# Optimization experiments

Measured on AMD Instinct MI355X. Metric: run time of the kernel, lower is better.

Reference implementation:

```python
import jax, jax.numpy as jnp
import numpy as np

# column-index constants for the node feature matrix and edge attributes
VM, VA, PG, QG, PD, QD = 0, 1, 2, 3, 4, 5
G_COL, B_COL = 0, 1

N_NODES = 100000
N_EDGES = 3200000
N_FEAT = 6


def setup_inputs() -> dict:
    key = jax.random.key(0)
    k1, k2, k3, k4, k5, k6 = jax.random.split(key, 6)
    pred = jax.random.normal(k1, (N_NODES, N_FEAT), dtype=jnp.float32)
    target = jax.random.normal(k2, (N_NODES, N_FEAT), dtype=jnp.float32)
    src = jax.random.randint(k3, (N_EDGES,), 0, N_NODES, dtype=jnp.int32)
    dst = jax.random.randint(k4, (N_EDGES,), 0, N_NODES, dtype=jnp.int32)
    edge_index = jnp.stack([src, dst], axis=0)
    edge_attr = jax.random.normal(k5, (N_EDGES, 2), dtype=jnp.float32)
    mask = jax.random.bernoulli(k6, 0.5, (N_NODES, N_FEAT))
    return {"pred": pred, "target": target, "edge_index": edge_index,
            "edge_attr": edge_attr, "mask": mask}


def reference(pred, target, edge_index, edge_attr, mask):
    # temp_pred[~mask] = target[~mask]
    tp = jnp.where(mask, pred, target)

    V_m = tp[:, VM]
    V_a = tp[:, VA]
    V = V_m * jnp.exp(1j * V_a)           # complex64 [N]
    V_conj = jnp.conj(V)

    # conj(Y_bus) entries on edges: G - jB
    Y_conj = edge_attr[:, G_COL] - 1j * edge_attr[:, B_COL]  # complex64 [E]

    row, col = edge_index[0], edge_index[1]
    # (Y_bus_conj @ V_conj)[i] = sum over edges (i,j) of conj(Y_ij) * conj(V_j)
    msg = Y_conj * V_conj[col]                               # gather-multiply [E]
    matvec = jax.ops.segment_sum(msg, row, num_segments=tp.shape[0])  # scatter-add [N]

    S_injection = V * matvec                                  # diag(V) @ (...)

    net_P = tp[:, PG] - tp[:, PD]
    net_Q = tp[:, QG] - tp[:, QD]
    diff = (net_P + 1j * net_Q) - S_injection

    loss = jnp.mean(jnp.abs(diff))
    real_loss = jnp.mean(jnp.abs(jnp.real(diff)))
    imag_loss = jnp.mean(jnp.abs(jnp.imag(diff)))
    return (loss, real_loss, imag_loss)
```

## Files before the change

### kernel.cpp

```cpp
#include <hip/hip_runtime.h>
#include <hip/hip_fp16.h>
#include <math.h>

constexpr int N_NODES = 100000;
constexpr int N_EDGES = 3200000;
constexpr int NF      = 6;

constexpr int BSHIFT  = 10;
constexpr int BNODES  = 1 << BSHIFT;
constexpr int NB      = (N_NODES + BNODES - 1) >> BSHIFT;
constexpr int CAP     = 33792;
constexpr int NSLICE  = 16;
constexpr int TILE    = 2048;
constexpr int EPT     = TILE / 256;
constexpr int NBLK_PART = (N_EDGES + TILE - 1) / TILE;
constexpr int VPREP_BLOCKS = (N_NODES + 255) / 256;

constexpr size_t OFF_V    = 0;
constexpr size_t OFF_REC  = OFF_V  + (size_t)N_NODES * 8;
constexpr size_t OFF_PART = OFF_REC + (size_t)NB * CAP * 8;
constexpr size_t OFF_CNT  = OFF_PART + (size_t)NB * NSLICE * BNODES * 8;
constexpr size_t WS_NEED  = OFF_CNT + 1024;

union F2U { float2 f; unsigned long long u; };

__device__ __forceinline__ float2 half2u_to_f2(unsigned u) {
    __half2 h;
    *reinterpret_cast<unsigned*>(&h) = u;
    return __half22float2(h);
}

__global__ __launch_bounds__(256) void partition_edges(
        const int* __restrict__ row, const int* __restrict__ col,
        const float2* __restrict__ attr,
        const float* __restrict__ pred, const float* __restrict__ target,
        const unsigned char* __restrict__ mask,
        float2* __restrict__ v_out,
        unsigned int* __restrict__ gcur,
        uint2* __restrict__ rec_g) {
    __shared__ unsigned int h[4][NB];
    __shared__ unsigned int cur[4][NB];
    __shared__ int wb[4][NB];
    __shared__ int dbase[NB];
    __shared__ unsigned int tot_s[NB];
    __shared__ uint2 rec_s[TILE];
    __shared__ unsigned char bkt_s[TILE];
    __shared__ int total_s;

    const int tid = threadIdx.x;
    const int w = tid >> 6;
    const int e0 = blockIdx.x * TILE;
    const int e_base = e0 + tid * EPT;
    const bool ok = e_base < N_EDGES;

    if (blockIdx.x < VPREP_BLOCKS) {
        int i = blockIdx.x * 256 + tid;
        if (i < N_NODES) {
            const int bb = i * NF;
            float vm = mask[bb + 0] ? pred[bb + 0] : target[bb + 0];
            float va = mask[bb + 1] ? pred[bb + 1] : target[bb + 1];
            float sn, cs;
            sincosf(va, &sn, &cs);
            v_out[i] = make_float2(vm * cs, vm * sn);
        }
    }

    for (int i = tid; i < 4 * NB; i += 256) {
        (&h[0][0])[i] = 0u;
        (&cur[0][0])[i] = 0u;
    }
    __syncthreads();

    int r[EPT];
    if (ok) {
        int4 ra = *(const int4*)(row + e_base);
        int4 rb = *(const int4*)(row + e_base + 4);
        r[0]=ra.x; r[1]=ra.y; r[2]=ra.z; r[3]=ra.w;
        r[4]=rb.x; r[5]=rb.y; r[6]=rb.z; r[7]=rb.w;
        #pragma unroll
        for (int k = 0; k < EPT; ++k)
            atomicAdd(&h[w][r[k] >> BSHIFT], 1u);
    }
    __syncthreads();

    if (tid < NB)
        tot_s[tid] = h[0][tid] + h[1][tid] + h[2][tid] + h[3][tid];
    __syncthreads();

    if (tid < NB) {
        int lbase = 0;
        for (int j = 0; j < tid; ++j) lbase += (int)tot_s[j];
        unsigned t0 = h[0][tid], t1 = h[1][tid], t2 = h[2][tid];
        unsigned tot = tot_s[tid];
        unsigned g = tot ? atomicAdd(&gcur[tid], tot) : 0u;
        dbase[tid] = (int)g - lbase;
        wb[0][tid] = lbase;
        wb[1][tid] = lbase + (int)t0;
        wb[2][tid] = lbase + (int)(t0 + t1);
        wb[3][tid] = lbase + (int)(t0 + t1 + t2);
        if (tid == NB - 1) total_s = lbase + (int)tot;
    }
    __syncthreads();

    if (ok) {
        int4 ca = *(const int4*)(col + e_base);
        int4 cb = *(const int4*)(col + e_base + 4);
        int c[EPT] = {ca.x, ca.y, ca.z, ca.w, cb.x, cb.y, cb.z, cb.w};
        float4 a0 = *(const float4*)(attr + e_base);
        float4 a1 = *(const float4*)(attr + e_base + 2);
        float4 a2 = *(const float4*)(attr + e_base + 4);
        float4 a3 = *(const float4*)(attr + e_base + 6);
        float gx[EPT] = {a0.x, a0.z, a1.x, a1.z, a2.x, a2.z, a3.x, a3.z};
        float gy[EPT] = {a0.y, a0.w, a1.y, a1.w, a2.y, a2.w, a3.y, a3.w};
        #pragma unroll
        for (int k = 0; k < EPT; ++k) {
            int rr = r[k];
            int b = rr >> BSHIFT;
            int slot = wb[w][b] + (int)atomicAdd(&cur[w][b], 1u);
            __half2 hh = __floats2half2_rn(gx[k], gy[k]);
            rec_s[slot] = make_uint2(
                (unsigned)c[k] | ((unsigned)(rr & (BNODES - 1)) << 17),
                *reinterpret_cast<unsigned int*>(&hh));
            bkt_s[slot] = (unsigned char)b;
        }
    }
    __syncthreads();

    const int total = total_s;
    for (int j = tid; j < total; j += 256) {
        int b = (int)bkt_s[j];
        int g = dbase[b] + j;
        if (g < CAP)
            rec_g[(size_t)b * CAP + g] = rec_s[j];
    }
}

__global__ __launch_bounds__(256) void accum_finalize(
        const unsigned int* __restrict__ gcur,
        const uint2* __restrict__ rec,
        unsigned long long* __restrict__ partials,
        unsigned int* __restrict__ sdone,
        float* __restrict__ sums,
        unsigned int* __restrict__ done_all,
        const float* __restrict__ pred,
        const float* __restrict__ target,
        const unsigned char* __restrict__ mask,
        const float2* __restrict__ v,
        float* __restrict__ out) {
    __shared__ float acc_re[BNODES];
    __shared__ float acc_im[BNODES];
    __shared__ unsigned int old_s;
    const int tid = threadIdx.x;
    const int b = blockIdx.x / NSLICE;
    const int s = blockIdx.x % NSLICE;
    int cnt = (int)min(gcur[b], (unsigned)CAP);
    for (int i = tid; i < BNODES; i += 256) { acc_re[i] = 0.f; acc_im[i] = 0.f; }
    __syncthreads();
    int per = (((cnt + NSLICE - 1) / NSLICE) + 3) & ~3;
    int st = s * per;
    int en = min(st + per, cnt);
    const uint2* rp = rec + (size_t)b * CAP;
    int j = st + 4 * tid;
    for (; j + 3 < en; j += 1024) {
        uint4 q0 = *(const uint4*)(rp + j);
        uint4 q1 = *(const uint4*)(rp + j + 2);
        int c0 = (int)(q0.x & 0x1FFFFu), li0 = (int)(q0.x >> 17);
        int c1 = (int)(q0.z & 0x1FFFFu), li1 = (int)(q0.z >> 17);
        int c2 = (int)(q1.x & 0x1FFFFu), li2 = (int)(q1.x >> 17);
        int c3 = (int)(q1.z & 0x1FFFFu), li3 = (int)(q1.z >> 17);
        float2 vv0 = v[c0];
        float2 vv1 = v[c1];
        float2 vv2 = v[c2];
        float2 vv3 = v[c3];
        float2 gb0 = half2u_to_f2(q0.y);
        float2 gb1 = half2u_to_f2(q0.w);
        float2 gb2 = half2u_to_f2(q1.y);
        float2 gb3 = half2u_to_f2(q1.w);
        atomicAdd(&acc_re[li0], fmaf(gb0.x, vv0.x, -gb0.y * vv0.y));
        atomicAdd(&acc_im[li0], -fmaf(gb0.x, vv0.y, gb0.y * vv0.x));
        atomicAdd(&acc_re[li1], fmaf(gb1.x, vv1.x, -gb1.y * vv1.y));
        atomicAdd(&acc_im[li1], -fmaf(gb1.x, vv1.y, gb1.y * vv1.x));
        atomicAdd(&acc_re[li2], fmaf(gb2.x, vv2.x, -gb2.y * vv2.y));
        atomicAdd(&acc_im[li2], -fmaf(gb2.x, vv2.y, gb2.y * vv2.x));
        atomicAdd(&acc_re[li3], fmaf(gb3.x, vv3.x, -gb3.y * vv3.y));
        atomicAdd(&acc_im[li3], -fmaf(gb3.x, vv3.y, gb3.y * vv3.x));
    }
    for (; j < en; ++j) {
        uint2 q = rp[j];
        int c0 = (int)(q.x & 0x1FFFFu), li0 = (int)(q.x >> 17);
        float2 vv0 = v[c0];
        float2 gb0 = half2u_to_f2(q.y);
        atomicAdd(&acc_re[li0], fmaf(gb0.x, vv0.x, -gb0.y * vv0.y));
        atomicAdd(&acc_im[li0], -fmaf(gb0.x, vv0.y, gb0.y * vv0.x));
    }
    __syncthreads();
    unsigned long long* p = partials + ((size_t)b * NSLICE + s) * BNODES;
    for (int i = tid; i < BNODES; i += 256) {
        F2U cvt;
        cvt.f = make_float2(acc_re[i], acc_im[i]);
        __hip_atomic_store(&p[i], cvt.u, __ATOMIC_RELAXED, __HIP_MEMORY_SCOPE_AGENT);
    }
    asm volatile("s_waitcnt vmcnt(0)" ::: "memory");
    __syncthreads();
    if (tid == 0)
        old_s = __hip_atomic_fetch_add(&sdone[b], 1u, __ATOMIC_RELAXED,
                                       __HIP_MEMORY_SCOPE_AGENT);
    __syncthreads();
    if (old_s != (unsigned)(NSLICE - 1)) return;

    const unsigned long long* pb = partials + (size_t)b * NSLICE * BNODES;
    float a = 0.f, ar = 0.f, ai = 0.f;
    for (int li = tid; li < BNODES; li += 256) {
        int i = (b << BSHIFT) + li;
        if (i >= N_NODES) break;
        float mr = 0.f, mi = 0.f;
        #pragma unroll
        for (int s2 = 0; s2 < NSLICE; ++s2) {
            F2U cvt;
            cvt.u = __hip_atomic_load(&pb[(size_t)s2 * BNODES + li],
                                      __ATOMIC_RELAXED, __HIP_MEMORY_SCOPE_AGENT);
            mr += cvt.f.x; mi += cvt.f.y;
        }
        const int bb = i * NF;
        float pg = mask[bb + 2] ? pred[bb + 2] : target[bb + 2];
        float qg = mask[bb + 3] ? pred[bb + 3] : target[bb + 3];
        float pd = mask[bb + 4] ? pred[bb + 4] : target[bb + 4];
        float qd = mask[bb + 5] ? pred[bb + 5] : target[bb + 5];
        float netP = pg - pd;
        float netQ = qg - qd;
        float2 vv = v[i];
        float s_re = vv.x * mr - vv.y * mi;
        float s_im = vv.x * mi + vv.y * mr;
        float dre = netP - s_re;
        float dim = netQ - s_im;
        ar += fabsf(dre);
        ai += fabsf(dim);
        a  += sqrtf(dre * dre + dim * dim);
    }
    #pragma unroll
    for (int off = 32; off > 0; off >>= 1) {
        a  += __shfl_down(a,  off, 64);
        ar += __shfl_down(ar, off, 64);
        ai += __shfl_down(ai, off, 64);
    }
    __shared__ float red[3][4];
    int wave = tid >> 6;
    int lane = tid & 63;
    if (lane == 0) { red[0][wave] = a; red[1][wave] = ar; red[2][wave] = ai; }
    __syncthreads();
    if (tid == 0) {
        float r0 = atomicAdd(&sums[0], red[0][0] + red[0][1] + red[0][2] + red[0][3]);
        float r1 = atomicAdd(&sums[1], red[1][0] + red[1][1] + red[1][2] + red[1][3]);
        float r2 = atomicAdd(&sums[2], red[2][0] + red[2][1] + red[2][2] + red[2][3]);
        float chk = r0 + r1 + r2;
        if (chk == chk) {
            unsigned fin = atomicAdd(done_all, 1u);
            if (fin == (unsigned)(NB - 1)) {
                const float inv = 1.0f / (float)N_NODES;
                float t0 = atomicAdd(&sums[0], 0.f);
                float t1 = atomicAdd(&sums[1], 0.f);
                float t2 = atomicAdd(&sums[2], 0.f);
                __hip_atomic_store(&out[0], t0 * inv, __ATOMIC_RELAXED, __HIP_MEMORY_SCOPE_AGENT);
                __hip_atomic_store(&out[1], t1 * inv, __ATOMIC_RELAXED, __HIP_MEMORY_SCOPE_AGENT);
                __hip_atomic_store(&out[2], t2 * inv, __ATOMIC_RELAXED, __HIP_MEMORY_SCOPE_AGENT);
            }
        }
    }
}

__global__ void node_prep_fb(const float* __restrict__ pred,
                             const float* __restrict__ target,
                             const unsigned char* __restrict__ mask,
                             float2* __restrict__ v) {
    int i = blockIdx.x * blockDim.x + threadIdx.x;
    if (i >= N_NODES) return;
    const int b = i * NF;
    float vm = mask[b + 0] ? pred[b + 0] : target[b + 0];
    float va = mask[b + 1] ? pred[b + 1] : target[b + 1];
    float s, c;
    sincosf(va, &s, &c);
    v[i] = make_float2(vm * c, vm * s);
}

__global__ void edge_scatter_fb(const int* __restrict__ row,
                                const int* __restrict__ col,
                                const float2* __restrict__ attr,
                                const float2* __restrict__ v,
                                float2* __restrict__ mv) {
    int e = blockIdx.x * blockDim.x + threadIdx.x;
    if (e >= N_EDGES) return;
    int r = row[e];
    int c = col[e];
    float2 gb = attr[e];
    float2 vv = v[c];
    float mre = fmaf(gb.x, vv.x, -gb.y * vv.y);
    float mim = -fmaf(gb.x, vv.y, gb.y * vv.x);
    atomicAdd(&mv[r].x, mre);
    atomicAdd(&mv[r].y, mim);
}

__global__ void finalize_fb(const float* __restrict__ pred,
                            const float* __restrict__ target,
                            const unsigned char* __restrict__ mask,
                            const float2* __restrict__ v,
                            const float2* __restrict__ mv,
                            float* __restrict__ sums) {
    int i = blockIdx.x * blockDim.x + threadIdx.x;
    float a = 0.f, ar = 0.f, ai = 0.f;
    if (i < N_NODES) {
        const int b = i * NF;
        float pg = mask[b + 2] ? pred[b + 2] : target[b + 2];
        float qg = mask[b + 3] ? pred[b + 3] : target[b + 3];
        float pd = mask[b + 4] ? pred[b + 4] : target[b + 4];
        float qd = mask[b + 5] ? pred[b + 5] : target[b + 5];
        float netP = pg - pd;
        float netQ = qg - qd;
        float2 vv = v[i];
        float2 m = mv[i];
        float s_re = vv.x * m.x - vv.y * m.y;
        float s_im = vv.x * m.y + vv.y * m.x;
        float dre = netP - s_re;
        float dim = netQ - s_im;
        ar = fabsf(dre);
        ai = fabsf(dim);
        a  = sqrtf(dre * dre + dim * dim);
    }
    #pragma unroll
    for (int off = 32; off > 0; off >>= 1) {
        a  += __shfl_down(a,  off, 64);
        ar += __shfl_down(ar, off, 64);
        ai += __shfl_down(ai, off, 64);
    }
    __shared__ float red[3][4];
    int wave = threadIdx.x >> 6;
    int lane = threadIdx.x & 63;
    if (lane == 0) { red[0][wave] = a; red[1][wave] = ar; red[2][wave] = ai; }
    __syncthreads();
    if (threadIdx.x == 0) {
        atomicAdd(&sums[0], red[0][0] + red[0][1] + red[0][2] + red[0][3]);
        atomicAdd(&sums[1], red[1][0] + red[1][1] + red[1][2] + red[1][3]);
        atomicAdd(&sums[2], red[2][0] + red[2][1] + red[2][2] + red[2][3]);
    }
}

__global__ void write_out_fb(const float* __restrict__ sums, float* __restrict__ out) {
    if (threadIdx.x == 0 && blockIdx.x == 0) {
        const float inv = 1.0f / (float)N_NODES;
        out[0] = sums[0] * inv;
        out[1] = sums[1] * inv;
        out[2] = sums[2] * inv;
    }
}

extern "C" void kernel_launch(void* const* d_in, const int* in_sizes, int n_in,
                              void* d_out, int out_size, void* d_ws, size_t ws_size,
                              hipStream_t stream) {
    const float*         pred   = (const float*)d_in[0];
    const float*         target = (const float*)d_in[1];
    const int*           eidx   = (const int*)d_in[2];
    const float2*        attr   = (const float2*)d_in[3];
    const unsigned char* mask   = (const unsigned char*)d_in[4];
    float* out = (float*)d_out;

    const int* row = eidx;
    const int* col = eidx + N_EDGES;

    char* ws = (char*)d_ws;
    const int B = 256;

    if (ws_size >= WS_NEED) {
        float2*             v        = (float2*)(ws + OFF_V);
        uint2*              rec_g    = (uint2*)(ws + OFF_REC);
        unsigned long long* partials = (unsigned long long*)(ws + OFF_PART);
        unsigned int*       gcur     = (unsigned int*)(ws + OFF_CNT);
        unsigned int*       sdone    = (unsigned int*)(ws + OFF_CNT + 512);
        float*              sums     = (float*)(ws + OFF_CNT + 912);
        unsigned int*       done_all = (unsigned int*)(ws + OFF_CNT + 928);

        hipMemsetAsync(ws + OFF_CNT, 0, 1024, stream);
        partition_edges<<<NBLK_PART, B, 0, stream>>>(row, col, attr,
                                                     pred, target, mask, v,
                                                     gcur, rec_g);
        accum_finalize<<<NB * NSLICE, B, 0, stream>>>(gcur, rec_g, partials,
                                                      sdone, sums, done_all,
                                                      pred, target, mask, v, out);
    } else {
        float2* v    = (float2*)ws;
        float2* mv   = (float2*)(ws + (size_t)N_NODES * 8);
        float*  sums = (float*)(ws + 2ull * N_NODES * 8);
        hipMemsetAsync(mv, 0, (size_t)N_NODES * 8 + 16, stream);
        node_prep_fb<<<(N_NODES + B - 1) / B, B, 0, stream>>>(pred, target, mask, v);
        edge_scatter_fb<<<(N_EDGES + B - 1) / B, B, 0, stream>>>(row, col, attr, v, mv);
        finalize_fb<<<(N_NODES + B - 1) / B, B, 0, stream>>>(pred, target, mask, v, mv, sums);
        write_out_fb<<<1, 64, 0, stream>>>(sums, out);
    }
}
```

Baseline: 183.8 us.

## Split accumulate and finalize into separate kernels instead of last-block reduction

```diff
diff --git a/kernel.cpp b/kernel.cpp
--- a/kernel.cpp
+++ b/kernel.cpp
@@ -15,14 +15,13 @@
 constexpr int EPT     = TILE / 256;
 constexpr int NBLK_PART = (N_EDGES + TILE - 1) / TILE;
 constexpr int VPREP_BLOCKS = (N_NODES + 255) / 256;
+constexpr int NBLK_FIN  = (N_NODES + 255) / 256;
 
 constexpr size_t OFF_V    = 0;
 constexpr size_t OFF_REC  = OFF_V  + (size_t)N_NODES * 8;
 constexpr size_t OFF_PART = OFF_REC + (size_t)NB * CAP * 8;
 constexpr size_t OFF_CNT  = OFF_PART + (size_t)NB * NSLICE * BNODES * 8;
 constexpr size_t WS_NEED  = OFF_CNT + 1024;
-
-union F2U { float2 f; unsigned long long u; };
 
 __device__ __forceinline__ float2 half2u_to_f2(unsigned u) {
     __half2 h;
@@ -135,21 +134,13 @@
     }
 }
 
-__global__ __launch_bounds__(256) void accum_finalize(
+__global__ __launch_bounds__(256) void accum_partials(
         const unsigned int* __restrict__ gcur,
         const uint2* __restrict__ rec,
-        unsigned long long* __restrict__ partials,
-        unsigned int* __restrict__ sdone,
-        float* __restrict__ sums,
-        unsigned int* __restrict__ done_all,
-        const float* __restrict__ pred,
-        const float* __restrict__ target,
-        const unsigned char* __restrict__ mask,
         const float2* __restrict__ v,
-        float* __restrict__ out) {
+        float2* __restrict__ partials) {
     __shared__ float acc_re[BNODES];
     __shared__ float acc_im[BNODES];
-    __shared__ unsigned int old_s;
     const int tid = threadIdx.x;
     const int b = blockIdx.x / NSLICE;
     const int s = blockIdx.x % NSLICE;
@@ -194,32 +185,34 @@
         atomicAdd(&acc_im[li0], -fmaf(gb0.x, vv0.y, gb0.y * vv0.x));
     }
     __syncthreads();
-    unsigned long long* p = partials + ((size_t)b * NSLICE + s) * BNODES;
-    for (int i = tid; i < BNODES; i += 256) {
-        F2U cvt;
-        cvt.f = make_float2(acc_re[i], acc_im[i]);
-        __hip_atomic_store(&p[i], cvt.u, __ATOMIC_RELAXED, __HIP_MEMORY_SCOPE_AGENT);
-    }
-    asm volatile("s_waitcnt vmcnt(0)" ::: "memory");
-    __syncthreads();
-    if (tid == 0)
-        old_s = __hip_atomic_fetch_add(&sdone[b], 1u, __ATOMIC_RELAXED,
-                                       __HIP_MEMORY_SCOPE_AGENT);
-    __syncthreads();
-    if (old_s != (unsigned)(NSLICE - 1)) return;
-
-    const unsigned long long* pb = partials + (size_t)b * NSLICE * BNODES;
+    float2* p = partials + ((size_t)b * NSLICE + s) * BNODES;
+    for (int i = 2 * tid; i < BNODES; i += 512) {
+        float4 q = make_float4(acc_re[i], acc_im[i], acc_re[i + 1], acc_im[i + 1]);
+        *(float4*)(p + i) = q;
+    }
+}
+
+__global__ __launch_bounds__(256) void finalize_nodes(
+        const float2* __restrict__ partials,
+        const float* __restrict__ pred,
+        const float* __restrict__ target,
+        const unsigned char* __restrict__ mask,
+        const float2* __restrict__ v,
+        float* __restrict__ sums,
+        unsigned int* __restrict__ done_all,
+        float* __restrict__ out) {
+    const int tid = threadIdx.x;
+    int i = blockIdx.x * 256 + tid;
     float a = 0.f, ar = 0.f, ai = 0.f;
-    for (int li = tid; li < BNODES; li += 256) {
-        int i = (b << BSHIFT) + li;
-        if (i >= N_NODES) break;
+    if (i < N_NODES) {
+        const int b = i >> BSHIFT;
+        const int li = i & (BNODES - 1);
+        const float2* pb = partials + (size_t)b * NSLICE * BNODES + li;
         float mr = 0.f, mi = 0.f;
         #pragma unroll
-        for (int s2 = 0; s2 < NSLICE; ++s2) {
-            F2U cvt;
-            cvt.u = __hip_atomic_load(&pb[(size_t)s2 * BNODES + li],
-                                      __ATOMIC_RELAXED, __HIP_MEMORY_SCOPE_AGENT);
-            mr += cvt.f.x; mi += cvt.f.y;
+        for (int s = 0; s < NSLICE; ++s) {
+            float2 pp = pb[(size_t)s * BNODES];
+            mr += pp.x; mi += pp.y;
         }
         const int bb = i * NF;
         float pg = mask[bb + 2] ? pred[bb + 2] : target[bb + 2];
@@ -233,9 +226,9 @@
         float s_im = vv.x * mi + vv.y * mr;
         float dre = netP - s_re;
         float dim = netQ - s_im;
-        ar += fabsf(dre);
-        ai += fabsf(dim);
-        a  += sqrtf(dre * dre + dim * dim);
+        ar = fabsf(dre);
+        ai = fabsf(dim);
+        a  = sqrtf(dre * dre + dim * dim);
     }
     #pragma unroll
     for (int off = 32; off > 0; off >>= 1) {
@@ -255,7 +248,7 @@
         float chk = r0 + r1 + r2;
         if (chk == chk) {
             unsigned fin = atomicAdd(done_all, 1u);
-            if (fin == (unsigned)(NB - 1)) {
+            if (fin == (unsigned)(NBLK_FIN - 1)) {
                 const float inv = 1.0f / (float)N_NODES;
                 float t0 = atomicAdd(&sums[0], 0.f);
                 float t1 = atomicAdd(&sums[1], 0.f);
@@ -369,21 +362,20 @@
     const int B = 256;
 
     if (ws_size >= WS_NEED) {
-        float2*             v        = (float2*)(ws + OFF_V);
-        uint2*              rec_g    = (uint2*)(ws + OFF_REC);
-        unsigned long long* partials = (unsigned long long*)(ws + OFF_PART);
-        unsigned int*       gcur     = (unsigned int*)(ws + OFF_CNT);
-        unsigned int*       sdone    = (unsigned int*)(ws + OFF_CNT + 512);
-        float*              sums     = (float*)(ws + OFF_CNT + 912);
-        unsigned int*       done_all = (unsigned int*)(ws + OFF_CNT + 928);
+        float2*       v        = (float2*)(ws + OFF_V);
+        uint2*        rec_g    = (uint2*)(ws + OFF_REC);
+        float2*       partials = (float2*)(ws + OFF_PART);
+        unsigned int* gcur     = (unsigned int*)(ws + OFF_CNT);
+        float*        sums     = (float*)(ws + OFF_CNT + 912);
+        unsigned int* done_all = (unsigned int*)(ws + OFF_CNT + 928);
 
         hipMemsetAsync(ws + OFF_CNT, 0, 1024, stream);
         partition_edges<<<NBLK_PART, B, 0, stream>>>(row, col, attr,
                                                      pred, target, mask, v,
                                                      gcur, rec_g);
-        accum_finalize<<<NB * NSLICE, B, 0, stream>>>(gcur, rec_g, partials,
-                                                      sdone, sums, done_all,
-                                                      pred, target, mask, v, out);
+        accum_partials<<<NB * NSLICE, B, 0, stream>>>(gcur, rec_g, v, partials);
+        finalize_nodes<<<NBLK_FIN, B, 0, stream>>>(partials, pred, target, mask, v,
+                                                   sums, done_all, out);
     } else {
         float2* v    = (float2*)ws;
         float2* mv   = (float2*)(ws + (size_t)N_NODES * 8);
```

After: 195.8 us. 1.07x slower.
